# Kernel tuning notes

Hardware: AMD Instinct MI355X
Metric: run time of the kernel (lower is better)

Reference implementation:

```python
import jax, jax.numpy as jnp
import numpy as np

NUM_HEADS = 16


def setup_inputs() -> dict:
    key = jax.random.key(0)
    k = jax.random.split(key, 5)
    b, s, h = 2, 2048, 1024
    scale = 1.0 / np.sqrt(h)
    return {
        "x": jax.random.normal(k[0], (b, s, h), dtype=jnp.float32),
        "W_qkv": jax.random.normal(k[1], (h, 3 * h), dtype=jnp.float32) * scale,
        "b_qkv": jax.random.normal(k[2], (3 * h,), dtype=jnp.float32) * 0.02,
        "W_o": jax.random.normal(k[3], (h, h), dtype=jnp.float32) * scale,
        "b_o": jax.random.normal(k[4], (h,), dtype=jnp.float32) * 0.02,
    }


def _mha_causal(Q, K, V, num_heads):
    b, s, hd = Q.shape
    d_head = hd // num_heads
    # b s (n h) -> b n s h
    _Q = Q.reshape(b, s, num_heads, d_head).transpose(0, 2, 1, 3)
    _K = K.reshape(b, s, num_heads, d_head).transpose(0, 2, 1, 3)
    _V = V.reshape(b, s, num_heads, d_head).transpose(0, 2, 1, 3)
    scores = jnp.einsum('bnqh,bnkh->bnqk', _Q, _K)
    causal = jnp.tril(jnp.ones((s, s), dtype=bool))  # True where allowed
    scores = jnp.where(causal, scores, -jnp.inf) / jnp.sqrt(jnp.float32(d_head))
    A = jax.nn.softmax(scores, axis=-1)
    AV = jnp.einsum('bnqk,bnkh->bnqh', A, _V)
    return AV.transpose(0, 2, 1, 3).reshape(b, s, hd)


def reference(x, W_qkv, b_qkv, W_o, b_o):
    qkv = x @ W_qkv + b_qkv  # [b, s, 3h]
    Q, K, V = jnp.split(qkv, 3, axis=-1)
    attn = _mha_causal(Q, K, V, NUM_HEADS)
    return attn @ W_o + b_o
```

## Files before the change

kernel.cpp:

```cpp
#include <hip/hip_runtime.h>
#include <hip/hip_bf16.h>

typedef unsigned short u16;
typedef __attribute__((ext_vector_type(8))) short short8;
typedef __attribute__((ext_vector_type(4))) float f32x4;
typedef __attribute__((ext_vector_type(16))) float f32x16;
typedef __attribute__((ext_vector_type(4))) float float4v;
typedef __attribute__((ext_vector_type(4))) unsigned int uint4v;
typedef __attribute__((ext_vector_type(2))) unsigned int uint2v;

__device__ __forceinline__ u16 f2bf(float f) {
    union { float f; unsigned u; } x;
    x.f = f;
    unsigned r = x.u + 0x7fffu + ((x.u >> 16) & 1u);
    return (u16)(r >> 16);
}

__device__ __forceinline__ unsigned cvtpk(float lo, float hi) {
    unsigned r;
    asm("v_cvt_pk_bf16_f32 %0, %1, %2" : "=v"(r) : "v"(lo), "v"(hi));
    return r;
}

__device__ __forceinline__ void gload16(const u16* g, u16* l) {
    __builtin_amdgcn_global_load_lds(
        (const __attribute__((address_space(1))) unsigned*)g,
        (__attribute__((address_space(3))) unsigned*)l, 16, 0, 0);
}

#define WAITV(n) asm volatile("s_waitcnt vmcnt(" #n ")" ::: "memory")

__global__ __launch_bounds__(256) void prep(
    const float* __restrict__ x, const float* __restrict__ Wqkv,
    const float* __restrict__ Wo, u16* __restrict__ x_bf,
    u16* __restrict__ wqkvT, u16* __restrict__ woT) {
    int bid = blockIdx.x;
    int t = threadIdx.x;
    if (bid < 2048) {
        int i = bid * 256 + t;
        const float4v* s = (const float4v*)(x + (size_t)i * 8);
        float4v a = s[0], b = s[1];
        uint4v o;
        o[0] = (unsigned)f2bf(a[0]) | ((unsigned)f2bf(a[1]) << 16);
        o[1] = (unsigned)f2bf(a[2]) | ((unsigned)f2bf(a[3]) << 16);
        o[2] = (unsigned)f2bf(b[0]) | ((unsigned)f2bf(b[1]) << 16);
        o[3] = (unsigned)f2bf(b[2]) | ((unsigned)f2bf(b[3]) << 16);
        *(uint4v*)(x_bf + (size_t)i * 8) = o;
        return;
    }
    const float* src;
    u16* dst;
    int C, tid;
    if (bid < 2816) { tid = bid - 2048; src = Wqkv; dst = wqkvT; C = 3072; }
    else            { tid = bid - 2816; src = Wo;   dst = woT;   C = 1024; }
    int tr = (tid & 15) * 64;
    int tc = (tid >> 4) * 64;
    __shared__ __align__(16) u16 tile[64][72];
    int r = t >> 2;
    int c4 = (t & 3) * 16;
    const float4v* sp = (const float4v*)(src + (size_t)(tr + r) * C + tc + c4);
#pragma unroll
    for (int v = 0; v < 4; v++) {
        float4v xv = sp[v];
#pragma unroll
        for (int j = 0; j < 4; j++) tile[r][c4 + v * 4 + j] = f2bf(xv[j]);
    }
    __syncthreads();
    u16* dp = dst + (size_t)(tc + r) * 1024 + tr + c4;
#pragma unroll
    for (int i = 0; i < 16; i++) dp[i] = tile[c4 + i][r];
}

__global__ __launch_bounds__(256) void gemm_qkv(
    const u16* __restrict__ A, const u16* __restrict__ BT,
    const float* __restrict__ bias, u16* __restrict__ qbuf,
    u16* __restrict__ kvp) {
    const int K = 1024;
    __shared__ __align__(16) u16 SMEM[24576];
    int bm = blockIdx.x, bn = blockIdx.y;
    int t = threadIdx.x;
    int lane = t & 63, wave = t >> 6;
    int wr = wave >> 1, wc = wave & 1;
    f32x4 acc[4][4] = {};

    const u16* gA = A + (size_t)(bm * 128) * K;
    const u16* gB = BT + (size_t)(bn * 128) * K;

    auto stage = [&](int buf, int k0) {
#pragma unroll
        for (int i = 0; i < 2; i++) {
            int o = i * 4096 + t * 16;
            int row = o >> 6;
            int cb = (o & 63) ^ (((row >> 1) & 3) << 4);
            gload16(gA + (size_t)row * K + k0 + (cb >> 1),
                    &SMEM[buf * 4096 + i * 2048 + (t & 192) * 8]);
        }
#pragma unroll
        for (int i = 0; i < 2; i++) {
            int o = i * 4096 + t * 16;
            int row = o >> 6;
            int cb = (o & 63) ^ (((row >> 1) & 3) << 4);
            gload16(gB + (size_t)row * K + k0 + (cb >> 1),
                    &SMEM[12288 + buf * 4096 + i * 2048 + (t & 192) * 8]);
        }
    };

    stage(0, 0);
    stage(1, 32);
    WAITV(4);
    __builtin_amdgcn_s_barrier();

    for (int tt = 0; tt < 32; tt++) {
        bool pre = (tt + 2 < 32);
        if (pre) stage((tt + 2) % 3, (tt + 2) << 5);
        int row16 = lane & 15;
        int colb = ((lane >> 4) * 16) ^ (((row16 >> 1) & 3) << 4);
        const u16* Ab = &SMEM[(tt % 3) * 4096];
        const u16* Bb = &SMEM[12288 + (tt % 3) * 4096];
        short8 af[4], bf[4];
#pragma unroll
        for (int m = 0; m < 4; m++)
            af[m] = *(const short8*)&Ab[(wr * 64 + m * 16 + row16) * 32 + (colb >> 1)];
#pragma unroll
        for (int n = 0; n < 4; n++)
            bf[n] = *(const short8*)&Bb[(wc * 64 + n * 16 + row16) * 32 + (colb >> 1)];
        __builtin_amdgcn_s_setprio(1);
#pragma unroll
        for (int m = 0; m < 4; m++)
#pragma unroll
            for (int n = 0; n < 4; n++)
                acc[m][n] = __builtin_amdgcn_mfma_f32_16x16x32_bf16(
                    af[m], bf[n], acc[m][n], 0, 0, 0);
        __builtin_amdgcn_s_setprio(0);
        if (pre) { WAITV(4); } else { WAITV(0); }
        __builtin_amdgcn_s_barrier();
    }

    int l15 = lane & 15, hi = lane >> 4;
    if (bn < 8) {
#pragma unroll
        for (int m = 0; m < 4; m++)
#pragma unroll
            for (int n = 0; n < 4; n++) {
                int col = bn * 128 + wc * 64 + n * 16 + l15;
                float bv = bias[col];
#pragma unroll
                for (int r = 0; r < 4; r++) {
                    int row = bm * 128 + wr * 64 + m * 16 + hi * 4 + r;
                    qbuf[(size_t)row * 1024 + col] = f2bf(acc[m][n][r] + bv);
                }
            }
    } else if (bn < 16) {
        int h2 = (bn - 8) * 2 + wc;
#pragma unroll
        for (int m = 0; m < 4; m++)
#pragma unroll
            for (int n = 0; n < 4; n++) {
                int d = n * 16 + l15;
                float bv = bias[1024 + h2 * 64 + d];
#pragma unroll
                for (int r = 0; r < 4; r++) {
                    int row = bm * 128 + wr * 64 + m * 16 + hi * 4 + r;
                    int b = row >> 11;
                    int tt = (row & 2047) >> 6;
                    int k = row & 63;
                    kvp[(size_t)(b * 16 + h2) * 262144 + tt * 8192 + k * 64 + d] =
                        f2bf(acc[m][n][r] + bv);
                }
            }
    } else {
        int h2 = (bn - 16) * 2 + wc;
        int rowbase = bm * 128 + wr * 64;
        int b = rowbase >> 11;
        int tt = (rowbase & 2047) >> 6;
        u16* wl = &SMEM[wave * 4608];
#pragma unroll
        for (int m = 0; m < 4; m++)
#pragma unroll
            for (int n = 0; n < 4; n++) {
                int d = n * 16 + l15;
                float bv = bias[2048 + h2 * 64 + d];
                unsigned p0 = cvtpk(acc[m][n][0] + bv, acc[m][n][1] + bv);
                unsigned p1 = cvtpk(acc[m][n][2] + bv, acc[m][n][3] + bv);
                *(uint2v*)&wl[d * 72 + m * 16 + hi * 4] = (uint2v){p0, p1};
            }
        u16* dst = kvp + (size_t)(b * 16 + h2) * 262144 + tt * 8192 + 4096;
#pragma unroll
        for (int i = 0; i < 8; i++)
            *(uint4v*)(dst + lane * 64 + i * 8) = *(const uint4v*)&wl[lane * 72 + i * 8];
    }
}

__global__ __launch_bounds__(256) void gemm_out(
    const u16* __restrict__ A, const u16* __restrict__ BT,
    const float* __restrict__ bias, float* __restrict__ Cout) {
    const int K = 1024, N = 1024;
    __shared__ __align__(16) u16 As[3][4096];
    __shared__ __align__(16) u16 Bs[3][2048];
    int bm = blockIdx.x, bn = blockIdx.y;
    int t = threadIdx.x;
    int lane = t & 63, wave = t >> 6;
    int wr = wave >> 1, wc = wave & 1;
    f32x4 acc[4][2] = {};

    const u16* gA = A + (size_t)(bm * 128) * K;
    const u16* gB = BT + (size_t)(bn * 64) * K;

    auto stage = [&](int buf, int k0) {
#pragma unroll
        for (int i = 0; i < 2; i++) {
            int o = i * 4096 + t * 16;
            int row = o >> 6;
            int cb = (o & 63) ^ (((row >> 1) & 3) << 4);
            gload16(gA + (size_t)row * K + k0 + (cb >> 1),
                    &As[buf][i * 2048 + (t & 192) * 8]);
        }
        {
            int o = t * 16;
            int row = o >> 6;
            int cb = (o & 63) ^ (((row >> 1) & 3) << 4);
            gload16(gB + (size_t)row * K + k0 + (cb >> 1),
                    &Bs[buf][(t & 192) * 8]);
        }
    };

    stage(0, 0);
    stage(1, 32);
    WAITV(3);
    __builtin_amdgcn_s_barrier();

    for (int tt = 0; tt < 32; tt++) {
        bool pre = (tt + 2 < 32);
        if (pre) stage((tt + 2) % 3, (tt + 2) << 5);
        int row16 = lane & 15;
        int colb = ((lane >> 4) * 16) ^ (((row16 >> 1) & 3) << 4);
        short8 af[4], bf[2];
#pragma unroll
        for (int m = 0; m < 4; m++)
            af[m] = *(const short8*)&As[tt % 3][(wr * 64 + m * 16 + row16) * 32 + (colb >> 1)];
#pragma unroll
        for (int n = 0; n < 2; n++)
            bf[n] = *(const short8*)&Bs[tt % 3][(wc * 32 + n * 16 + row16) * 32 + (colb >> 1)];
        __builtin_amdgcn_s_setprio(1);
#pragma unroll
        for (int m = 0; m < 4; m++)
#pragma unroll
            for (int n = 0; n < 2; n++)
                acc[m][n] = __builtin_amdgcn_mfma_f32_16x16x32_bf16(
                    af[m], bf[n], acc[m][n], 0, 0, 0);
        __builtin_amdgcn_s_setprio(0);
        if (pre) { WAITV(3); } else { WAITV(0); }
        __builtin_amdgcn_s_barrier();
    }

#pragma unroll
    for (int m = 0; m < 4; m++)
#pragma unroll
        for (int n = 0; n < 2; n++) {
            int col = bn * 64 + wc * 32 + n * 16 + (lane & 15);
            float bv = bias[col];
#pragma unroll
            for (int r = 0; r < 4; r++) {
                int row = bm * 128 + wr * 64 + m * 16 + (lane >> 4) * 4 + r;
                Cout[(size_t)row * N + col] = acc[m][n][r] + bv;
            }
        }
}

__global__ __launch_bounds__(256, 2) void attn_kernel(
    const u16* __restrict__ qbuf, const u16* __restrict__ kvp,
    u16* __restrict__ attn, float* __restrict__ part_o,
    float* __restrict__ part_l) {
    int bid = blockIdx.x;
    int bh = bid & 31;
    int j = 23 - (bid >> 5);
    int sp, tbeg, tend, kc = 0;
    bool partial;
    if (j >= 8) {
        int idx = j - 8;
        sp = 8 + (idx >> 1);
        kc = idx & 1;
        int half = sp + 1;
        partial = true;
        tbeg = kc ? half : 0;
        tend = kc ? 2 * sp + 2 : half;
    } else {
        sp = j;
        partial = false;
        tbeg = 0;
        tend = 2 * sp + 2;
    }
    int b = bh >> 4, h = bh & 15;
    int t = threadIdx.x;
    int lane = t & 63, w = t >> 6;
    int qb = sp * 128 + w * 32;
    int kend = qb + 32;
    int l31 = lane & 31, hi32 = lane >> 5;
    int swz = (lane & 7) << 4;

    __shared__ __align__(16) u16 KVb[24576];

    const u16* kvb = kvp + (size_t)bh * 262144;

    auto stage = [&](int buf, int tt) {
        const char* g0 = (const char*)(kvb + (size_t)tt * 8192);
#pragma unroll
        for (int kv2 = 0; kv2 < 2; kv2++)
#pragma unroll
            for (int i = 0; i < 2; i++) {
                int o = i * 4096 + t * 16;
                int row = o >> 7;
                int cb = (o & 127) ^ ((row & 7) << 4);
                gload16((const u16*)(g0 + kv2 * 8192 + row * 128 + cb),
                        &KVb[buf * 8192 + kv2 * 4096 + i * 2048 + (t & 192) * 8]);
            }
    };

    short8 qf[4];
    {
        const u16* q0 = qbuf + (size_t)(b * 2048 + qb + l31) * 1024 + h * 64 + hi32 * 8;
#pragma unroll
        for (int dd = 0; dd < 4; dd++) qf[dd] = *(const short8*)(q0 + dd * 16);
    }
    stage(tbeg % 3, tbeg);
    stage((tbeg + 1) % 3, tbeg + 1);

    float l_lane = 0.f;
    f32x16 oT[2] = {};

    const float C1 = 0.1803368880f;
    const float C2 = -17.3123404907f;

    WAITV(4);
    __builtin_amdgcn_s_barrier();

    for (int tt = tbeg; tt < tend; tt++) {
        bool pre = (tt + 2 < tend);
        if (pre) stage((tt + 2) % 3, tt + 2);
        int k0 = tt * 64;
        if (k0 < kend) {
            const u16* Ks = &KVb[(tt % 3) * 8192];
            const u16* Vs = Ks + 4096;
            f32x16 sc[2];
            __builtin_amdgcn_s_setprio(1);
#pragma unroll
            for (int kb = 0; kb < 2; kb++) {
                f32x16 z = {};
#pragma unroll
                for (int dd = 0; dd < 4; dd++) {
                    int off = (kb * 32 + l31) * 64 + (((dd * 32 + hi32 * 16) ^ swz) >> 1);
                    short8 kf = *(const short8*)&Ks[off];
                    z = __builtin_amdgcn_mfma_f32_32x32x16_bf16(kf, qf[dd], z, 0, 0, 0);
                }
                sc[kb] = z;
            }
            __builtin_amdgcn_s_setprio(0);

            float p[2][16];
            int q_g = qb + l31;
            if (k0 + 64 > qb) {
#pragma unroll
                for (int kb = 0; kb < 2; kb++)
#pragma unroll
                    for (int r = 0; r < 16; r++) {
                        int kg = k0 + kb * 32 + (r & 3) + 8 * (r >> 2) + 4 * hi32;
                        float v = (kg <= q_g) ? sc[kb][r] : -1e30f;
                        float pe = __builtin_amdgcn_exp2f(fmaf(v, C1, C2));
                        p[kb][r] = pe;
                        l_lane += pe;
                    }
            } else {
#pragma unroll
                for (int kb = 0; kb < 2; kb++)
#pragma unroll
                    for (int r = 0; r < 16; r++) {
                        float pe = __builtin_amdgcn_exp2f(fmaf(sc[kb][r], C1, C2));
                        p[kb][r] = pe;
                        l_lane += pe;
                    }
            }

            short8 pb[4];
#pragma unroll
            for (int kb = 0; kb < 2; kb++)
#pragma unroll
                for (int cset = 0; cset < 2; cset++) {
                    const float* pp = &p[kb][cset * 8];
                    unsigned A0 = cvtpk(pp[0], pp[1]);
                    unsigned A1 = cvtpk(pp[2], pp[3]);
                    unsigned A2 = cvtpk(pp[4], pp[5]);
                    unsigned A3 = cvtpk(pp[6], pp[7]);
                    unsigned za = hi32 ? A0 : A2;
                    unsigned zb = hi32 ? A1 : A3;
                    unsigned sa = (unsigned)__shfl_xor((int)za, 32, 64);
                    unsigned sb = (unsigned)__shfl_xor((int)zb, 32, 64);
                    uint4v wv;
                    wv[0] = hi32 ? sa : A0;
                    wv[1] = hi32 ? sb : A1;
                    wv[2] = hi32 ? A2 : sa;
                    wv[3] = hi32 ? A3 : sb;
                    pb[kb * 2 + cset] = __builtin_bit_cast(short8, wv);
                }

            __builtin_amdgcn_s_setprio(1);
#pragma unroll
            for (int mb = 0; mb < 2; mb++)
#pragma unroll
                for (int kk = 0; kk < 4; kk++) {
                    int off = (mb * 32 + l31) * 64 + (((kk * 32 + hi32 * 16) ^ swz) >> 1);
                    short8 vf = *(const short8*)&Vs[off];
                    oT[mb] = __builtin_amdgcn_mfma_f32_32x32x16_bf16(vf, pb[kk], oT[mb], 0, 0, 0);
                }
            __builtin_amdgcn_s_setprio(0);
        }
        if (pre) { WAITV(4); } else { WAITV(0); }
        __builtin_amdgcn_s_barrier();
    }

    if (partial) {
        int blk = (bh * 8 + (sp - 8)) * 2 + kc;
        float* po = part_o + (size_t)blk * 8192;
        int lr = w * 32 + l31;
        float lf = l_lane + __shfl_xor(l_lane, 32, 64);
        if (hi32 == 0) part_l[blk * 128 + lr] = lf;
#pragma unroll
        for (int mb = 0; mb < 2; mb++)
#pragma unroll
            for (int r = 0; r < 16; r++) {
                int d = mb * 32 + (r & 3) + 8 * (r >> 2) + 4 * hi32;
                po[lr * 64 + d] = oT[mb][r];
            }
        return;
    }

    float lf = l_lane + __shfl_xor(l_lane, 32, 64);
    float linv = __builtin_amdgcn_rcpf(lf);
    u16* gp = attn + (size_t)(b * 2048 + qb + l31) * 1024 + h * 64;
#pragma unroll
    for (int mb = 0; mb < 2; mb++)
#pragma unroll
        for (int g = 0; g < 4; g++) {
            unsigned w0 = cvtpk(oT[mb][4 * g] * linv, oT[mb][4 * g + 1] * linv);
            unsigned w1 = cvtpk(oT[mb][4 * g + 2] * linv, oT[mb][4 * g + 3] * linv);
            int d0 = mb * 32 + g * 8 + hi32 * 4;
            *(uint2v*)(gp + d0) = (uint2v){w0, w1};
        }
}

__global__ __launch_bounds__(256) void attn_merge(
    const float* __restrict__ part_o, const float* __restrict__ part_l,
    u16* __restrict__ attn) {
    int bid = blockIdx.x;
    int bh = bid & 31;
    int sp8 = bid >> 5;
    int sp = sp8 + 8;
    int b = bh >> 4, h = bh & 15;
    int t = threadIdx.x;
    int blk0 = (bh * 8 + sp8) * 2;
    const float* o0 = part_o + (size_t)blk0 * 8192;
    const float* o1 = o0 + 8192;
    const float* l0 = part_l + blk0 * 128;
    const float* l1 = l0 + 128;
#pragma unroll
    for (int i = 0; i < 4; i++) {
        int r = (t >> 3) + i * 32;
        int d0 = (t & 7) * 8;
        float linv = __builtin_amdgcn_rcpf(l0[r] + l1[r]);
        const float* a = o0 + r * 64 + d0;
        const float* c = o1 + r * 64 + d0;
        uint4v w;
#pragma unroll
        for (int k = 0; k < 4; k++)
            w[k] = cvtpk((a[2 * k] + c[2 * k]) * linv,
                         (a[2 * k + 1] + c[2 * k + 1]) * linv);
        u16* gp = attn + (size_t)(b * 2048 + sp * 128 + r) * 1024 + h * 64 + d0;
        *(uint4v*)gp = w;
    }
}

extern "C" void kernel_launch(void* const* d_in, const int* in_sizes, int n_in,
                              void* d_out, int out_size, void* d_ws, size_t ws_size,
                              hipStream_t stream) {
    const float* x    = (const float*)d_in[0];
    const float* Wqkv = (const float*)d_in[1];
    const float* bqkv = (const float*)d_in[2];
    const float* Wo   = (const float*)d_in[3];
    const float* bo   = (const float*)d_in[4];
    float* out = (float*)d_out;

    char* ws = (char*)d_ws;
    u16* x_bf   = (u16*)(ws);
    u16* attnb  = (u16*)(ws);
    u16* wqkvT  = (u16*)(ws + (8ull << 20));
    u16* woT    = (u16*)(ws + (14ull << 20));
    u16* qbuf   = (u16*)(ws + (16ull << 20));
    u16* kvp    = (u16*)(ws + (24ull << 20));
    float* part_o = (float*)(ws + (40ull << 20));
    float* part_l = (float*)(ws + (56ull << 20));

    prep<<<3072, 256, 0, stream>>>(x, Wqkv, Wo, x_bf, wqkvT, woT);
    gemm_qkv<<<dim3(32, 24), 256, 0, stream>>>(x_bf, wqkvT, bqkv, qbuf, kvp);
    attn_kernel<<<768, 256, 0, stream>>>(qbuf, kvp, attnb, part_o, part_l);
    attn_merge<<<256, 256, 0, stream>>>(part_o, part_l, attnb);
    gemm_out<<<dim3(32, 16), 256, 0, stream>>>(attnb, woT, bo, out);
}
```

Baseline: 109.3 us.

## Transpose MFMA operands for vectorized epilogue stores and load V directly from global

In the QKV and output GEMMs the MFMA operands are swapped for Q/K and output tiles, so each lane holds four consecutive columns and the epilogue can do vector bias loads and packed 8- or 16-byte stores instead of scalar stores. The V epilogue drops its LDS transpose staging and writes directly to global. The attention kernel now stages only K in LDS, loads V fragments straight from global into registers, and interleaves the P packing with the PV MFMAs. Its occupancy hint of 2 is removed and partial-output stores are vectorized. The attention changes trade LDS traffic and footprint for more register pressure and uncached global latency on V.

```diff
diff --git a/kernel.cpp b/kernel.cpp
--- a/kernel.cpp
+++ b/kernel.cpp
@@ -81,6 +81,7 @@
     int t = threadIdx.x;
     int lane = t & 63, wave = t >> 6;
     int wr = wave >> 1, wc = wave & 1;
+    bool doswap = (bn < 16);
     f32x4 acc[4][4] = {};
 
     const u16* gA = A + (size_t)(bm * 128) * K;
@@ -125,12 +126,21 @@
         for (int n = 0; n < 4; n++)
             bf[n] = *(const short8*)&Bb[(wc * 64 + n * 16 + row16) * 32 + (colb >> 1)];
         __builtin_amdgcn_s_setprio(1);
-#pragma unroll
-        for (int m = 0; m < 4; m++)
-#pragma unroll
-            for (int n = 0; n < 4; n++)
-                acc[m][n] = __builtin_amdgcn_mfma_f32_16x16x32_bf16(
-                    af[m], bf[n], acc[m][n], 0, 0, 0);
+        if (doswap) {
+#pragma unroll
+            for (int m = 0; m < 4; m++)
+#pragma unroll
+                for (int n = 0; n < 4; n++)
+                    acc[m][n] = __builtin_amdgcn_mfma_f32_16x16x32_bf16(
+                        bf[n], af[m], acc[m][n], 0, 0, 0);
+        } else {
+#pragma unroll
+            for (int m = 0; m < 4; m++)
+#pragma unroll
+                for (int n = 0; n < 4; n++)
+                    acc[m][n] = __builtin_amdgcn_mfma_f32_16x16x32_bf16(
+                        af[m], bf[n], acc[m][n], 0, 0, 0);
+        }
         __builtin_amdgcn_s_setprio(0);
         if (pre) { WAITV(4); } else { WAITV(0); }
         __builtin_amdgcn_s_barrier();
@@ -142,52 +152,51 @@
         for (int m = 0; m < 4; m++)
 #pragma unroll
             for (int n = 0; n < 4; n++) {
-                int col = bn * 128 + wc * 64 + n * 16 + l15;
-                float bv = bias[col];
-#pragma unroll
-                for (int r = 0; r < 4; r++) {
-                    int row = bm * 128 + wr * 64 + m * 16 + hi * 4 + r;
-                    qbuf[(size_t)row * 1024 + col] = f2bf(acc[m][n][r] + bv);
-                }
+                int col0 = bn * 128 + wc * 64 + n * 16 + hi * 4;
+                float4v bv = *(const float4v*)&bias[col0];
+                int row = bm * 128 + wr * 64 + m * 16 + l15;
+                uint2v w;
+                w[0] = cvtpk(acc[m][n][0] + bv[0], acc[m][n][1] + bv[1]);
+                w[1] = cvtpk(acc[m][n][2] + bv[2], acc[m][n][3] + bv[3]);
+                *(uint2v*)(qbuf + (size_t)row * 1024 + col0) = w;
             }
     } else if (bn < 16) {
         int h2 = (bn - 8) * 2 + wc;
 #pragma unroll
-        for (int m = 0; m < 4; m++)
+        for (int m = 0; m < 4; m++) {
+            int row = bm * 128 + wr * 64 + m * 16 + l15;
+            int b = row >> 11;
+            int tv = (row & 2047) >> 6;
+            int k = row & 63;
+            u16* kb = kvp + (size_t)(b * 16 + h2) * 262144 + tv * 8192 + k * 64;
 #pragma unroll
             for (int n = 0; n < 4; n++) {
-                int d = n * 16 + l15;
-                float bv = bias[1024 + h2 * 64 + d];
-#pragma unroll
-                for (int r = 0; r < 4; r++) {
-                    int row = bm * 128 + wr * 64 + m * 16 + hi * 4 + r;
-                    int b = row >> 11;
-                    int tt = (row & 2047) >> 6;
-                    int k = row & 63;
-                    kvp[(size_t)(b * 16 + h2) * 262144 + tt * 8192 + k * 64 + d] =
-                        f2bf(acc[m][n][r] + bv);
-                }
+                int d0 = n * 16 + hi * 4;
+                float4v bv = *(const float4v*)&bias[1024 + h2 * 64 + d0];
+                uint2v w;
+                w[0] = cvtpk(acc[m][n][0] + bv[0], acc[m][n][1] + bv[1]);
+                w[1] = cvtpk(acc[m][n][2] + bv[2], acc[m][n][3] + bv[3]);
+                *(uint2v*)(kb + d0) = w;
             }
+        }
     } else {
         int h2 = (bn - 16) * 2 + wc;
         int rowbase = bm * 128 + wr * 64;
         int b = rowbase >> 11;
-        int tt = (rowbase & 2047) >> 6;
-        u16* wl = &SMEM[wave * 4608];
+        int tv = (rowbase & 2047) >> 6;
+        u16* vb = kvp + (size_t)(b * 16 + h2) * 262144 + tv * 8192 + 4096;
 #pragma unroll
         for (int m = 0; m < 4; m++)
 #pragma unroll
             for (int n = 0; n < 4; n++) {
                 int d = n * 16 + l15;
                 float bv = bias[2048 + h2 * 64 + d];
-                unsigned p0 = cvtpk(acc[m][n][0] + bv, acc[m][n][1] + bv);
-                unsigned p1 = cvtpk(acc[m][n][2] + bv, acc[m][n][3] + bv);
-                *(uint2v*)&wl[d * 72 + m * 16 + hi * 4] = (uint2v){p0, p1};
+                int k0 = m * 16 + hi * 4;
+                uint2v w;
+                w[0] = cvtpk(acc[m][n][0] + bv, acc[m][n][1] + bv);
+                w[1] = cvtpk(acc[m][n][2] + bv, acc[m][n][3] + bv);
+                *(uint2v*)(vb + d * 64 + k0) = w;
             }
-        u16* dst = kvp + (size_t)(b * 16 + h2) * 262144 + tt * 8192 + 4096;
-#pragma unroll
-        for (int i = 0; i < 8; i++)
-            *(uint4v*)(dst + lane * 64 + i * 8) = *(const uint4v*)&wl[lane * 72 + i * 8];
     }
 }
 
@@ -247,27 +256,27 @@
 #pragma unroll
             for (int n = 0; n < 2; n++)
                 acc[m][n] = __builtin_amdgcn_mfma_f32_16x16x32_bf16(
-                    af[m], bf[n], acc[m][n], 0, 0, 0);
+                    bf[n], af[m], acc[m][n], 0, 0, 0);
         __builtin_amdgcn_s_setprio(0);
         if (pre) { WAITV(3); } else { WAITV(0); }
         __builtin_amdgcn_s_barrier();
     }
 
+    int l15 = lane & 15, hi = lane >> 4;
 #pragma unroll
     for (int m = 0; m < 4; m++)
 #pragma unroll
         for (int n = 0; n < 2; n++) {
-            int col = bn * 64 + wc * 32 + n * 16 + (lane & 15);
-            float bv = bias[col];
-#pragma unroll
-            for (int r = 0; r < 4; r++) {
-                int row = bm * 128 + wr * 64 + m * 16 + (lane >> 4) * 4 + r;
-                Cout[(size_t)row * N + col] = acc[m][n][r] + bv;
-            }
-        }
-}
-
-__global__ __launch_bounds__(256, 2) void attn_kernel(
+            int col0 = bn * 64 + wc * 32 + n * 16 + hi * 4;
+            float4v bv = *(const float4v*)&bias[col0];
+            int row = bm * 128 + wr * 64 + m * 16 + l15;
+            float4v v = {acc[m][n][0] + bv[0], acc[m][n][1] + bv[1],
+                         acc[m][n][2] + bv[2], acc[m][n][3] + bv[3]};
+            *(float4v*)(Cout + (size_t)row * N + col0) = v;
+        }
+}
+
+__global__ __launch_bounds__(256) void attn_kernel(
     const u16* __restrict__ qbuf, const u16* __restrict__ kvp,
     u16* __restrict__ attn, float* __restrict__ part_o,
     float* __restrict__ part_l) {
@@ -298,22 +307,20 @@
     int l31 = lane & 31, hi32 = lane >> 5;
     int swz = (lane & 7) << 4;
 
-    __shared__ __align__(16) u16 KVb[24576];
+    __shared__ __align__(16) u16 Ks[3][4096];
 
     const u16* kvb = kvp + (size_t)bh * 262144;
 
-    auto stage = [&](int buf, int tt) {
+    auto stageK = [&](int buf, int tt) {
         const char* g0 = (const char*)(kvb + (size_t)tt * 8192);
 #pragma unroll
-        for (int kv2 = 0; kv2 < 2; kv2++)
-#pragma unroll
-            for (int i = 0; i < 2; i++) {
-                int o = i * 4096 + t * 16;
-                int row = o >> 7;
-                int cb = (o & 127) ^ ((row & 7) << 4);
-                gload16((const u16*)(g0 + kv2 * 8192 + row * 128 + cb),
-                        &KVb[buf * 8192 + kv2 * 4096 + i * 2048 + (t & 192) * 8]);
-            }
+        for (int i = 0; i < 2; i++) {
+            int o = i * 4096 + t * 16;
+            int row = o >> 7;
+            int cb = (o & 127) ^ ((row & 7) << 4);
+            gload16((const u16*)(g0 + row * 128 + cb),
+                    &Ks[buf][i * 2048 + (t & 192) * 8]);
+        }
     };
 
     short8 qf[4];
@@ -322,8 +329,8 @@
 #pragma unroll
         for (int dd = 0; dd < 4; dd++) qf[dd] = *(const short8*)(q0 + dd * 16);
     }
-    stage(tbeg % 3, tbeg);
-    stage((tbeg + 1) % 3, tbeg + 1);
+    stageK(tbeg % 3, tbeg);
+    stageK((tbeg + 1) % 3, tbeg + 1);
 
     float l_lane = 0.f;
     f32x16 oT[2] = {};
@@ -331,16 +338,26 @@
     const float C1 = 0.1803368880f;
     const float C2 = -17.3123404907f;
 
-    WAITV(4);
+    WAITV(2);
     __builtin_amdgcn_s_barrier();
 
     for (int tt = tbeg; tt < tend; tt++) {
         bool pre = (tt + 2 < tend);
-        if (pre) stage((tt + 2) % 3, tt + 2);
         int k0 = tt * 64;
-        if (k0 < kend) {
-            const u16* Ks = &KVb[(tt % 3) * 8192];
-            const u16* Vs = Ks + 4096;
+        bool active = (k0 < kend);
+        short8 vf[2][4];
+        if (active) {
+            const u16* vp = kvb + (size_t)tt * 8192 + 4096;
+#pragma unroll
+            for (int mb = 0; mb < 2; mb++)
+#pragma unroll
+                for (int kk = 0; kk < 4; kk++)
+                    vf[mb][kk] = *(const short8*)(vp + (mb * 32 + l31) * 64 +
+                                                  kk * 16 + hi32 * 8);
+        }
+        if (pre) stageK((tt + 2) % 3, tt + 2);
+        if (active) {
+            const u16* Ksb = Ks[tt % 3];
             f32x16 sc[2];
             __builtin_amdgcn_s_setprio(1);
 #pragma unroll
@@ -349,14 +366,13 @@
 #pragma unroll
                 for (int dd = 0; dd < 4; dd++) {
                     int off = (kb * 32 + l31) * 64 + (((dd * 32 + hi32 * 16) ^ swz) >> 1);
-                    short8 kf = *(const short8*)&Ks[off];
+                    short8 kf = *(const short8*)&Ksb[off];
                     z = __builtin_amdgcn_mfma_f32_32x32x16_bf16(kf, qf[dd], z, 0, 0, 0);
                 }
                 sc[kb] = z;
             }
             __builtin_amdgcn_s_setprio(0);
 
-            float p[2][16];
             int q_g = qb + l31;
             if (k0 + 64 > qb) {
 #pragma unroll
@@ -366,7 +382,7 @@
                         int kg = k0 + kb * 32 + (r & 3) + 8 * (r >> 2) + 4 * hi32;
                         float v = (kg <= q_g) ? sc[kb][r] : -1e30f;
                         float pe = __builtin_amdgcn_exp2f(fmaf(v, C1, C2));
-                        p[kb][r] = pe;
+                        sc[kb][r] = pe;
                         l_lane += pe;
                     }
             } else {
@@ -375,21 +391,21 @@
 #pragma unroll
                     for (int r = 0; r < 16; r++) {
                         float pe = __builtin_amdgcn_exp2f(fmaf(sc[kb][r], C1, C2));
-                        p[kb][r] = pe;
+                        sc[kb][r] = pe;
                         l_lane += pe;
                     }
             }
 
-            short8 pb[4];
+            __builtin_amdgcn_s_setprio(1);
 #pragma unroll
             for (int kb = 0; kb < 2; kb++)
 #pragma unroll
                 for (int cset = 0; cset < 2; cset++) {
-                    const float* pp = &p[kb][cset * 8];
-                    unsigned A0 = cvtpk(pp[0], pp[1]);
-                    unsigned A1 = cvtpk(pp[2], pp[3]);
-                    unsigned A2 = cvtpk(pp[4], pp[5]);
-                    unsigned A3 = cvtpk(pp[6], pp[7]);
+                    int kk = kb * 2 + cset;
+                    unsigned A0 = cvtpk(sc[kb][cset * 8 + 0], sc[kb][cset * 8 + 1]);
+                    unsigned A1 = cvtpk(sc[kb][cset * 8 + 2], sc[kb][cset * 8 + 3]);
+                    unsigned A2 = cvtpk(sc[kb][cset * 8 + 4], sc[kb][cset * 8 + 5]);
+                    unsigned A3 = cvtpk(sc[kb][cset * 8 + 6], sc[kb][cset * 8 + 7]);
                     unsigned za = hi32 ? A0 : A2;
                     unsigned zb = hi32 ? A1 : A3;
                     unsigned sa = (unsigned)__shfl_xor((int)za, 32, 64);
@@ -399,21 +415,13 @@
                     wv[1] = hi32 ? sb : A1;
                     wv[2] = hi32 ? A2 : sa;
                     wv[3] = hi32 ? A3 : sb;
-                    pb[kb * 2 + cset] = __builtin_bit_cast(short8, wv);
-                }
-
-            __builtin_amdgcn_s_setprio(1);
-#pragma unroll
-            for (int mb = 0; mb < 2; mb++)
-#pragma unroll
-                for (int kk = 0; kk < 4; kk++) {
-                    int off = (mb * 32 + l31) * 64 + (((kk * 32 + hi32 * 16) ^ swz) >> 1);
-                    short8 vf = *(const short8*)&Vs[off];
-                    oT[mb] = __builtin_amdgcn_mfma_f32_32x32x16_bf16(vf, pb[kk], oT[mb], 0, 0, 0);
+                    short8 pb = __builtin_bit_cast(short8, wv);
+                    oT[0] = __builtin_amdgcn_mfma_f32_32x32x16_bf16(vf[0][kk], pb, oT[0], 0, 0, 0);
+                    oT[1] = __builtin_amdgcn_mfma_f32_32x32x16_bf16(vf[1][kk], pb, oT[1], 0, 0, 0);
                 }
             __builtin_amdgcn_s_setprio(0);
         }
-        if (pre) { WAITV(4); } else { WAITV(0); }
+        if (pre) { WAITV(2); } else { WAITV(0); }
         __builtin_amdgcn_s_barrier();
     }
 
@@ -426,9 +434,11 @@
 #pragma unroll
         for (int mb = 0; mb < 2; mb++)
 #pragma unroll
-            for (int r = 0; r < 16; r++) {
-                int d = mb * 32 + (r & 3) + 8 * (r >> 2) + 4 * hi32;
-                po[lr * 64 + d] = oT[mb][r];
+            for (int g = 0; g < 4; g++) {
+                int d0 = mb * 32 + g * 8 + hi32 * 4;
+                f32x4 v = {oT[mb][4 * g], oT[mb][4 * g + 1],
+                           oT[mb][4 * g + 2], oT[mb][4 * g + 3]};
+                *(f32x4*)(po + lr * 64 + d0) = v;
             }
         return;
     }
```

Result: slower. 159.1 us (+45.6%).
